# Kernel optimization log

Measured on AMD Instinct MI355X. Metric: run time of the kernel, lower is better.

## Reference

```python
import jax, jax.numpy as jnp
import numpy as np

C = 343.0      # speed of sound (init kwarg c)
F = 16         # number of frequency channels (len(omega))
H = 128        # MLP hidden width
N = 131072     # collocation points


def _mlp(coords, W1, b1, W2, b2, W3, b3):
    # coords: [..., 3] -> [..., 2F] (first F = real part, last F = imag part)
    h = jnp.tanh(coords @ W1 + b1)
    h = jnp.tanh(h @ W2 + b2)
    return h @ W3 + b3


def setup_inputs() -> dict:
    key = jax.random.key(0)
    ks = jax.random.split(key, 4)
    inputs = jax.random.normal(ks[0], (N, 3), dtype=jnp.float32)
    # omega = 2*pi*f for f = 100..1600 Hz (matches init kwarg list)
    omega = 2.0 * jnp.pi * 100.0 * jnp.arange(1, F + 1, dtype=jnp.float32)
    s_in = 1.0 / np.sqrt(3.0)
    s_h = 1.0 / np.sqrt(float(H))
    W1 = jax.random.normal(ks[1], (3, H), dtype=jnp.float32) * s_in
    b1 = jnp.zeros((H,), dtype=jnp.float32)
    W2 = jax.random.normal(ks[2], (H, H), dtype=jnp.float32) * s_h
    b2 = jnp.zeros((H,), dtype=jnp.float32)
    W3 = jax.random.normal(ks[3], (H, 2 * F), dtype=jnp.float32) * s_h
    b3 = jnp.zeros((2 * F,), dtype=jnp.float32)
    return {"inputs": inputs, "omega": omega, "W1": W1, "b1": b1,
            "W2": W2, "b2": b2, "W3": W3, "b3": b3}


def reference(inputs, omega, W1, b1, W2, b2, W3, b3):
    # Pointwise network R^3 -> R^{2F} (real/imag stacked).
    f = lambda c3: _mlp(c3, W1, b1, W2, b2, W3, b3)

    # u: complex pressure per point per frequency, [N, F]
    out = _mlp(inputs, W1, b1, W2, b2, W3, b3)           # [N, 2F]
    u = out[:, :F] + 1j * out[:, F:]

    # Full spatial Hessian per point via forward-over-reverse AD (fused
    # replacement for the torch per-channel autograd.grad loop).
    hess = jax.vmap(jax.jacfwd(jax.jacrev(f)))(inputs)   # [N, 2F, 3, 3]
    lap_ri = jnp.einsum('nfii->nf', hess)                # diagonal trace = Laplacian
    lap = lap_ri[:, :F] + 1j * lap_ri[:, F:]             # [N, F] complex

    # PDE residual skips channel 0, exactly as the torch loop (i+1 indexing).
    k2 = (omega[1:] / C) ** 2                            # [F-1]
    residual = lap[:, 1:] + k2 * u[:, 1:]                # [N, F-1]

    # mean over channels then over batch == global mean of |residual|^2
    return jnp.mean(jnp.abs(residual) ** 2)
```

## Files before the change

kernel.cpp:

```cpp
#include <hip/hip_runtime.h>
#include <math.h>

#ifndef __has_builtin
#define __has_builtin(x) 0
#endif

#define NPTS   131072
#define FCH    16
#define CSND   343.0f
#define PB     32
#define BLOCK  256
#define GRID   512
#define NBLK   (NPTS / PB)

typedef _Float16 half8 __attribute__((ext_vector_type(8)));
typedef _Float16 half2v __attribute__((ext_vector_type(2)));
typedef float    f32x4 __attribute__((ext_vector_type(4)));

static __device__ __forceinline__ unsigned pack2(float a, float b) {
#if __has_builtin(__builtin_amdgcn_cvt_pkrtz)
  return __builtin_bit_cast(unsigned, __builtin_amdgcn_cvt_pkrtz(a, b));
#else
  half2v v; v[0] = (_Float16)a; v[1] = (_Float16)b;
  return __builtin_bit_cast(unsigned, v);
#endif
}

static __device__ __forceinline__ float mytanh(float x) {
#if __has_builtin(__builtin_amdgcn_exp2f)
  float e = __builtin_amdgcn_exp2f(2.885390082f * x);
#else
  float e = __expf(2.0f * x);
#endif
  return fmaf(-2.0f, __builtin_amdgcn_rcpf(e + 1.0f), 1.0f);
}


__global__ __launch_bounds__(BLOCK, 2) void helmholtz_kernel(
    const float* __restrict__ x,
    const float* __restrict__ omega,
    const float* __restrict__ W1,
    const float* __restrict__ b1,
    const float* __restrict__ W2,
    const float* __restrict__ b2,
    const float* __restrict__ W3,
    const float* __restrict__ b3,
    float* __restrict__ out)
{
  __shared__ unsigned s_A[160 * 64];
  __shared__ unsigned s_HG[32 * 128];

  const int tid  = threadIdx.x;
  const int w    = tid >> 6;
  const int l    = tid & 63;
  const int col  = l & 15;
  const int quad = l >> 4;
  const int ph   = w >> 1;
  const int nh   = w & 1;

  const int pA = tid >> 4;
  const int g  = tid & 15;
  float wx[8], wy[8], wz[8], bB[8], wq[8];
#pragma unroll
  for (int u = 0; u < 8; u++) {
    int unit = 8 * g + u;
    wx[u] = W1[unit]; wy[u] = W1[128 + unit]; wz[u] = W1[256 + unit];
    bB[u] = b1[unit];
    wq[u] = wx[u] * wx[u] + wy[u] * wy[u] + wz[u] * wz[u];
  }

  half8 w2f[4][4];
#pragma unroll
  for (int t4 = 0; t4 < 4; t4++) {
    const int n = 64 * nh + 16 * t4 + col;
#pragma unroll
    for (int ks = 0; ks < 4; ks++) {
      half8 f;
#pragma unroll
      for (int j8 = 0; j8 < 8; j8++)
        f[j8] = (_Float16)W2[(ks * 32 + (quad << 3) + j8) * 128 + n];
      w2f[t4][ks] = f;
    }
  }
  half8 w3f[4];
#pragma unroll
  for (int ks = 0; ks < 4; ks++) {
    half8 f;
#pragma unroll
    for (int j8 = 0; j8 < 8; j8++) {
      int kap = ks * 32 + (quad << 3) + j8;
      int q   = kap >> 1;
      int j   = 64 * (q >> 5) + 32 * ((q >> 4) & 1) + 16 * (kap & 1) + (q & 15);
      f[j8] = (_Float16)W3[j * 32 + 16 * nh + col];
    }
    w3f[ks] = f;
  }

  float b2r[4];
#pragma unroll
  for (int t4 = 0; t4 < 4; t4++) b2r[t4] = b2[64 * nh + 16 * t4 + col];
  float k2v = 0.0f;
  if (col >= 1) {
    float om = omega[col] * (1.0f / CSND);
    k2v = om * om;
  }
  const float b3v = b3[16 * nh + col];

  float wsum = 0.0f;
  float xr[2][3];

  auto loadX = [&](int blk) {
    const float* xb = x + (size_t)blk * PB * 3;
#pragma unroll
    for (int hp = 0; hp < 2; hp++) {
      int p = pA + 16 * hp;
      xr[hp][0] = xb[3 * p]; xr[hp][1] = xb[3 * p + 1]; xr[hp][2] = xb[3 * p + 2];
    }
  };

  auto phaseA = [&]() {
    const int cbase = (g ^ pA) << 2;
#pragma unroll
    for (int hp = 0; hp < 2; hp++) {
      int p = pA + 16 * hp;
      float x0 = xr[hp][0], x1 = xr[hp][1], x2 = xr[hp][2];
      float t[8], s[8];
#pragma unroll
      for (int u = 0; u < 8; u++) {
        float z = fmaf(x0, wx[u], fmaf(x1, wy[u], fmaf(x2, wz[u], bB[u])));
        t[u] = mytanh(z);
        s[u] = 1.0f - t[u] * t[u];
      }
      uint4 q;
      q = make_uint4(pack2(t[0], t[1]), pack2(t[2], t[3]),
                     pack2(t[4], t[5]), pack2(t[6], t[7]));
      *(uint4*)&s_A[(p)       * 64 + cbase] = q;
      q = make_uint4(pack2(s[0]*wx[0], s[1]*wx[1]), pack2(s[2]*wx[2], s[3]*wx[3]),
                     pack2(s[4]*wx[4], s[5]*wx[5]), pack2(s[6]*wx[6], s[7]*wx[7]));
      *(uint4*)&s_A[(32 + p)  * 64 + cbase] = q;
      q = make_uint4(pack2(s[0]*wy[0], s[1]*wy[1]), pack2(s[2]*wy[2], s[3]*wy[3]),
                     pack2(s[4]*wy[4], s[5]*wy[5]), pack2(s[6]*wy[6], s[7]*wy[7]));
      *(uint4*)&s_A[(64 + p)  * 64 + cbase] = q;
      q = make_uint4(pack2(s[0]*wz[0], s[1]*wz[1]), pack2(s[2]*wz[2], s[3]*wz[3]),
                     pack2(s[4]*wz[4], s[5]*wz[5]), pack2(s[6]*wz[6], s[7]*wz[7]));
      *(uint4*)&s_A[(96 + p)  * 64 + cbase] = q;
      float c[8];
#pragma unroll
      for (int u = 0; u < 8; u++) c[u] = -2.0f * t[u] * s[u] * wq[u];
      q = make_uint4(pack2(c[0], c[1]), pack2(c[2], c[3]),
                     pack2(c[4], c[5]), pack2(c[6], c[7]));
      *(uint4*)&s_A[(128 + p) * 64 + cbase] = q;
    }
  };

  auto phaseDE = [&]() {
    const int pbase = (16 * ph + col) * 128;
    f32x4 dy = (f32x4){0.0f, 0.0f, 0.0f, 0.0f};
    f32x4 dl = (f32x4){0.0f, 0.0f, 0.0f, 0.0f};
#pragma unroll
    for (int ks = 0; ks < 4; ks++) {
      int pos = ((((ks << 2) + quad) ^ col) << 2);
      half8 afy = *(const half8*)&s_HG[pbase + pos];
      half8 afl = *(const half8*)&s_HG[pbase + 64 + pos];
      dy = __builtin_amdgcn_mfma_f32_16x16x32_f16(afy, w3f[ks], dy, 0, 0, 0);
      dl = __builtin_amdgcn_mfma_f32_16x16x32_f16(afl, w3f[ks], dl, 0, 0, 0);
    }
    if (col >= 1) {
#pragma unroll
      for (int r = 0; r < 4; r++) {
        float yv  = dy[r] + b3v;
        float res = fmaf(k2v, yv, dl[r]);
        wsum += res * res;
      }
    }
  };

  loadX(blockIdx.x);
  bool first = true;
  for (int blk = blockIdx.x; blk < NBLK; blk += gridDim.x) {
    if (!first) phaseDE();
    first = false;
    phaseA();
    __syncthreads();

    int nblk = blk + (int)gridDim.x;
    if (nblk < NBLK) loadX(nblk);

    f32x4 acc[5][4];
#pragma unroll
    for (int v = 0; v < 5; v++)
#pragma unroll
      for (int t4 = 0; t4 < 4; t4++)
        acc[v][t4] = (f32x4){0.0f, 0.0f, 0.0f, 0.0f};

#pragma unroll
    for (int v = 0; v < 5; v++) {
      const int rb = (v * 32 + 16 * ph + col) * 64;
#pragma unroll
      for (int ks = 0; ks < 4; ks++) {
        half8 af = *(const half8*)&s_A[rb + ((((ks << 2) + quad) ^ col) << 2)];
        acc[v][0] = __builtin_amdgcn_mfma_f32_16x16x32_f16(af, w2f[0][ks], acc[v][0], 0, 0, 0);
        acc[v][1] = __builtin_amdgcn_mfma_f32_16x16x32_f16(af, w2f[1][ks], acc[v][1], 0, 0, 0);
        acc[v][2] = __builtin_amdgcn_mfma_f32_16x16x32_f16(af, w2f[2][ks], acc[v][2], 0, 0, 0);
        acc[v][3] = __builtin_amdgcn_mfma_f32_16x16x32_f16(af, w2f[3][ks], acc[v][3], 0, 0, 0);
      }
    }

#pragma unroll
    for (int r = 0; r < 4; r++) {
      int p = 16 * ph + (quad << 2) + r;
      float t2[4], gg[4];
#pragma unroll
      for (int t4 = 0; t4 < 4; t4++) {
        float z2 = acc[0][t4][r] + b2r[t4];
        float d0 = acc[1][t4][r], d1 = acc[2][t4][r], d2 = acc[3][t4][r];
        float Av = acc[4][t4][r];
        float t  = mytanh(z2);
        float s2 = 1.0f - t * t;
        t2[t4] = t;
        gg[t4] = s2 * (Av - 2.0f * t * (d0 * d0 + d1 * d1 + d2 * d2));
      }
      int pb = p * 128;
#pragma unroll
      for (int pr = 0; pr < 2; pr++) {
        int q   = 32 * nh + 16 * pr + col;
        int pos = (((q >> 2) ^ (p & 15)) << 2) + (q & 3);
        s_HG[pb + pos]      = pack2(t2[2 * pr], t2[2 * pr + 1]);
        s_HG[pb + 64 + pos] = pack2(gg[2 * pr], gg[2 * pr + 1]);
      }
    }
    __syncthreads();
  }
  phaseDE();

#pragma unroll
  for (int off = 32; off > 0; off >>= 1)
    wsum += __shfl_down(wsum, off, 64);
  if (l == 0)
    atomicAdd(out, wsum * (1.0f / ((float)NPTS * (float)(FCH - 1))));
}

extern "C" void kernel_launch(void* const* d_in, const int* in_sizes, int n_in,
                              void* d_out, int out_size, void* d_ws, size_t ws_size,
                              hipStream_t stream) {
  const float* x     = (const float*)d_in[0];
  const float* omega = (const float*)d_in[1];
  const float* W1    = (const float*)d_in[2];
  const float* b1    = (const float*)d_in[3];
  const float* W2    = (const float*)d_in[4];
  const float* b2    = (const float*)d_in[5];
  const float* W3    = (const float*)d_in[6];
  const float* b3    = (const float*)d_in[7];
  float* out = (float*)d_out;

  (void)hipMemsetAsync(out, 0, sizeof(float), stream);
  helmholtz_kernel<<<GRID, BLOCK, 0, stream>>>(x, omega, W1, b1, W2, b2, W3, b3, out);
}
```

Baseline: 124.4 us.

## Halve points per block and split hidden units across waves for higher occupancy

Each block now handles 16 points instead of 32. The 128 hidden units of layer 2 are split across all four waves, so each wave holds half as many W2 fragments and accumulators. Shared memory and register use drop, so launch bounds allow three blocks per CU and the grid grows to 768. In exchange, only two of the four waves do the output-layer phase, W3 is re-indexed to match, and the per-block barrier and setup overhead is spread over fewer points.

```diff
diff --git a/kernel.cpp b/kernel.cpp
--- a/kernel.cpp
+++ b/kernel.cpp
@@ -8,9 +8,9 @@
 #define NPTS   131072
 #define FCH    16
 #define CSND   343.0f
-#define PB     32
+#define PB     16
 #define BLOCK  256
-#define GRID   512
+#define GRID   768
 #define NBLK   (NPTS / PB)
 
 typedef _Float16 half8 __attribute__((ext_vector_type(8)));
@@ -36,7 +36,7 @@
 }
 
 
-__global__ __launch_bounds__(BLOCK, 2) void helmholtz_kernel(
+__global__ __launch_bounds__(BLOCK, 3) void helmholtz_kernel(
     const float* __restrict__ x,
     const float* __restrict__ omega,
     const float* __restrict__ W1,
@@ -47,39 +47,37 @@
     const float* __restrict__ b3,
     float* __restrict__ out)
 {
-  __shared__ unsigned s_A[160 * 64];
-  __shared__ unsigned s_HG[32 * 128];
+  __shared__ unsigned s_A[80 * 64];
+  __shared__ unsigned s_HG[16 * 128];
 
   const int tid  = threadIdx.x;
   const int w    = tid >> 6;
   const int l    = tid & 63;
   const int col  = l & 15;
   const int quad = l >> 4;
-  const int ph   = w >> 1;
   const int nh   = w & 1;
 
   const int pA = tid >> 4;
   const int g  = tid & 15;
-  float wx[8], wy[8], wz[8], bB[8], wq[8];
+  float wx[8], wy[8], wz[8], bB[8];
 #pragma unroll
   for (int u = 0; u < 8; u++) {
     int unit = 8 * g + u;
     wx[u] = W1[unit]; wy[u] = W1[128 + unit]; wz[u] = W1[256 + unit];
     bB[u] = b1[unit];
-    wq[u] = wx[u] * wx[u] + wy[u] * wy[u] + wz[u] * wz[u];
-  }
-
-  half8 w2f[4][4];
-#pragma unroll
-  for (int t4 = 0; t4 < 4; t4++) {
-    const int n = 64 * nh + 16 * t4 + col;
+  }
+
+  half8 w2f[2][4];
+#pragma unroll
+  for (int ntl = 0; ntl < 2; ntl++) {
+    const int n = 32 * w + 16 * ntl + col;
 #pragma unroll
     for (int ks = 0; ks < 4; ks++) {
       half8 f;
 #pragma unroll
       for (int j8 = 0; j8 < 8; j8++)
         f[j8] = (_Float16)W2[(ks * 32 + (quad << 3) + j8) * 128 + n];
-      w2f[t4][ks] = f;
+      w2f[ntl][ks] = f;
     }
   }
   half8 w3f[4];
@@ -90,15 +88,14 @@
     for (int j8 = 0; j8 < 8; j8++) {
       int kap = ks * 32 + (quad << 3) + j8;
       int q   = kap >> 1;
-      int j   = 64 * (q >> 5) + 32 * ((q >> 4) & 1) + 16 * (kap & 1) + (q & 15);
+      int j   = 32 * (q >> 4) + 16 * (kap & 1) + (q & 15);
       f[j8] = (_Float16)W3[j * 32 + 16 * nh + col];
     }
     w3f[ks] = f;
   }
 
-  float b2r[4];
-#pragma unroll
-  for (int t4 = 0; t4 < 4; t4++) b2r[t4] = b2[64 * nh + 16 * t4 + col];
+  const float b2r0 = b2[32 * w + col];
+  const float b2r1 = b2[32 * w + 16 + col];
   float k2v = 0.0f;
   if (col >= 1) {
     float om = omega[col] * (1.0f / CSND);
@@ -107,54 +104,48 @@
   const float b3v = b3[16 * nh + col];
 
   float wsum = 0.0f;
-  float xr[2][3];
+  float xr0, xr1, xr2;
 
   auto loadX = [&](int blk) {
-    const float* xb = x + (size_t)blk * PB * 3;
-#pragma unroll
-    for (int hp = 0; hp < 2; hp++) {
-      int p = pA + 16 * hp;
-      xr[hp][0] = xb[3 * p]; xr[hp][1] = xb[3 * p + 1]; xr[hp][2] = xb[3 * p + 2];
-    }
+    const float* xp = x + (size_t)(blk * PB + pA) * 3;
+    xr0 = xp[0]; xr1 = xp[1]; xr2 = xp[2];
   };
 
   auto phaseA = [&]() {
     const int cbase = (g ^ pA) << 2;
-#pragma unroll
-    for (int hp = 0; hp < 2; hp++) {
-      int p = pA + 16 * hp;
-      float x0 = xr[hp][0], x1 = xr[hp][1], x2 = xr[hp][2];
-      float t[8], s[8];
-#pragma unroll
-      for (int u = 0; u < 8; u++) {
-        float z = fmaf(x0, wx[u], fmaf(x1, wy[u], fmaf(x2, wz[u], bB[u])));
-        t[u] = mytanh(z);
-        s[u] = 1.0f - t[u] * t[u];
-      }
-      uint4 q;
-      q = make_uint4(pack2(t[0], t[1]), pack2(t[2], t[3]),
-                     pack2(t[4], t[5]), pack2(t[6], t[7]));
-      *(uint4*)&s_A[(p)       * 64 + cbase] = q;
-      q = make_uint4(pack2(s[0]*wx[0], s[1]*wx[1]), pack2(s[2]*wx[2], s[3]*wx[3]),
-                     pack2(s[4]*wx[4], s[5]*wx[5]), pack2(s[6]*wx[6], s[7]*wx[7]));
-      *(uint4*)&s_A[(32 + p)  * 64 + cbase] = q;
-      q = make_uint4(pack2(s[0]*wy[0], s[1]*wy[1]), pack2(s[2]*wy[2], s[3]*wy[3]),
-                     pack2(s[4]*wy[4], s[5]*wy[5]), pack2(s[6]*wy[6], s[7]*wy[7]));
-      *(uint4*)&s_A[(64 + p)  * 64 + cbase] = q;
-      q = make_uint4(pack2(s[0]*wz[0], s[1]*wz[1]), pack2(s[2]*wz[2], s[3]*wz[3]),
-                     pack2(s[4]*wz[4], s[5]*wz[5]), pack2(s[6]*wz[6], s[7]*wz[7]));
-      *(uint4*)&s_A[(96 + p)  * 64 + cbase] = q;
-      float c[8];
-#pragma unroll
-      for (int u = 0; u < 8; u++) c[u] = -2.0f * t[u] * s[u] * wq[u];
-      q = make_uint4(pack2(c[0], c[1]), pack2(c[2], c[3]),
-                     pack2(c[4], c[5]), pack2(c[6], c[7]));
-      *(uint4*)&s_A[(128 + p) * 64 + cbase] = q;
-    }
+    float t[8], s[8];
+#pragma unroll
+    for (int u = 0; u < 8; u++) {
+      float z = fmaf(xr0, wx[u], fmaf(xr1, wy[u], fmaf(xr2, wz[u], bB[u])));
+      t[u] = mytanh(z);
+      s[u] = 1.0f - t[u] * t[u];
+    }
+    uint4 q;
+    q = make_uint4(pack2(t[0], t[1]), pack2(t[2], t[3]),
+                   pack2(t[4], t[5]), pack2(t[6], t[7]));
+    *(uint4*)&s_A[(pA)      * 64 + cbase] = q;
+    q = make_uint4(pack2(s[0]*wx[0], s[1]*wx[1]), pack2(s[2]*wx[2], s[3]*wx[3]),
+                   pack2(s[4]*wx[4], s[5]*wx[5]), pack2(s[6]*wx[6], s[7]*wx[7]));
+    *(uint4*)&s_A[(16 + pA) * 64 + cbase] = q;
+    q = make_uint4(pack2(s[0]*wy[0], s[1]*wy[1]), pack2(s[2]*wy[2], s[3]*wy[3]),
+                   pack2(s[4]*wy[4], s[5]*wy[5]), pack2(s[6]*wy[6], s[7]*wy[7]));
+    *(uint4*)&s_A[(32 + pA) * 64 + cbase] = q;
+    q = make_uint4(pack2(s[0]*wz[0], s[1]*wz[1]), pack2(s[2]*wz[2], s[3]*wz[3]),
+                   pack2(s[4]*wz[4], s[5]*wz[5]), pack2(s[6]*wz[6], s[7]*wz[7]));
+    *(uint4*)&s_A[(48 + pA) * 64 + cbase] = q;
+    float c[8];
+#pragma unroll
+    for (int u = 0; u < 8; u++) {
+      float wq = fmaf(wx[u], wx[u], fmaf(wy[u], wy[u], wz[u] * wz[u]));
+      c[u] = -2.0f * t[u] * s[u] * wq;
+    }
+    q = make_uint4(pack2(c[0], c[1]), pack2(c[2], c[3]),
+                   pack2(c[4], c[5]), pack2(c[6], c[7]));
+    *(uint4*)&s_A[(64 + pA) * 64 + cbase] = q;
   };
 
   auto phaseDE = [&]() {
-    const int pbase = (16 * ph + col) * 128;
+    const int pbase = col * 128;
     f32x4 dy = (f32x4){0.0f, 0.0f, 0.0f, 0.0f};
     f32x4 dl = (f32x4){0.0f, 0.0f, 0.0f, 0.0f};
 #pragma unroll
@@ -178,7 +169,7 @@
   loadX(blockIdx.x);
   bool first = true;
   for (int blk = blockIdx.x; blk < NBLK; blk += gridDim.x) {
-    if (!first) phaseDE();
+    if (!first && w < 2) phaseDE();
     first = false;
     phaseA();
     __syncthreads();
@@ -186,52 +177,46 @@
     int nblk = blk + (int)gridDim.x;
     if (nblk < NBLK) loadX(nblk);
 
-    f32x4 acc[5][4];
+    f32x4 acc[5][2];
 #pragma unroll
     for (int v = 0; v < 5; v++)
 #pragma unroll
-      for (int t4 = 0; t4 < 4; t4++)
-        acc[v][t4] = (f32x4){0.0f, 0.0f, 0.0f, 0.0f};
+      for (int ntl = 0; ntl < 2; ntl++)
+        acc[v][ntl] = (f32x4){0.0f, 0.0f, 0.0f, 0.0f};
 
 #pragma unroll
     for (int v = 0; v < 5; v++) {
-      const int rb = (v * 32 + 16 * ph + col) * 64;
+      const int rb = (v * 16 + col) * 64;
 #pragma unroll
       for (int ks = 0; ks < 4; ks++) {
         half8 af = *(const half8*)&s_A[rb + ((((ks << 2) + quad) ^ col) << 2)];
         acc[v][0] = __builtin_amdgcn_mfma_f32_16x16x32_f16(af, w2f[0][ks], acc[v][0], 0, 0, 0);
         acc[v][1] = __builtin_amdgcn_mfma_f32_16x16x32_f16(af, w2f[1][ks], acc[v][1], 0, 0, 0);
-        acc[v][2] = __builtin_amdgcn_mfma_f32_16x16x32_f16(af, w2f[2][ks], acc[v][2], 0, 0, 0);
-        acc[v][3] = __builtin_amdgcn_mfma_f32_16x16x32_f16(af, w2f[3][ks], acc[v][3], 0, 0, 0);
       }
     }
 
 #pragma unroll
     for (int r = 0; r < 4; r++) {
-      int p = 16 * ph + (quad << 2) + r;
-      float t2[4], gg[4];
-#pragma unroll
-      for (int t4 = 0; t4 < 4; t4++) {
-        float z2 = acc[0][t4][r] + b2r[t4];
-        float d0 = acc[1][t4][r], d1 = acc[2][t4][r], d2 = acc[3][t4][r];
-        float Av = acc[4][t4][r];
+      int p = (quad << 2) + r;
+      float t2[2], gg[2];
+#pragma unroll
+      for (int ntl = 0; ntl < 2; ntl++) {
+        float z2 = acc[0][ntl][r] + (ntl ? b2r1 : b2r0);
+        float d0 = acc[1][ntl][r], d1 = acc[2][ntl][r], d2 = acc[3][ntl][r];
+        float Av = acc[4][ntl][r];
         float t  = mytanh(z2);
         float s2 = 1.0f - t * t;
-        t2[t4] = t;
-        gg[t4] = s2 * (Av - 2.0f * t * (d0 * d0 + d1 * d1 + d2 * d2));
+        t2[ntl] = t;
+        gg[ntl] = s2 * (Av - 2.0f * t * (d0 * d0 + d1 * d1 + d2 * d2));
       }
-      int pb = p * 128;
-#pragma unroll
-      for (int pr = 0; pr < 2; pr++) {
-        int q   = 32 * nh + 16 * pr + col;
-        int pos = (((q >> 2) ^ (p & 15)) << 2) + (q & 3);
-        s_HG[pb + pos]      = pack2(t2[2 * pr], t2[2 * pr + 1]);
-        s_HG[pb + 64 + pos] = pack2(gg[2 * pr], gg[2 * pr + 1]);
-      }
+      int q   = 16 * w + col;
+      int pos = (((q >> 2) ^ p) << 2) + (q & 3);
+      s_HG[p * 128 + pos]      = pack2(t2[0], t2[1]);
+      s_HG[p * 128 + 64 + pos] = pack2(gg[0], gg[1]);
     }
     __syncthreads();
   }
-  phaseDE();
+  if (w < 2) phaseDE();
 
 #pragma unroll
   for (int off = 32; off > 0; off >>= 1)
```

Result: slower. 128.7 us (+3.5%).
